# Kernel optimization log

Measured on AMD Instinct MI355X. Metric: run time of the kernel, lower is better.

## Reference

```python
import jax, jax.numpy as jnp
import numpy as np

NUM_HEADS = 12


def setup_inputs() -> dict:
    key = jax.random.key(0)
    k1, k2, k3 = jax.random.split(key, 3)
    B, S, D = 2, 2048, 768
    x = jax.random.normal(k1, (B, S, D), dtype=jnp.float32)
    # torch Linear init: normal(std=0.002) weights, zero bias; stored as [in, out]
    W_qkv = jax.random.normal(k2, (D, 3 * D), dtype=jnp.float32) * 0.002
    b_qkv = jnp.zeros((3 * D,), dtype=jnp.float32)
    W_vw = jax.random.normal(k3, (D, D), dtype=jnp.float32) * 0.002
    b_vw = jnp.zeros((D,), dtype=jnp.float32)
    mask = jnp.ones((B, S), dtype=jnp.int32)  # padding mask, all valid
    return {"x": x, "W_qkv": W_qkv, "b_qkv": b_qkv, "W_vw": W_vw, "b_vw": b_vw, "mask": mask}


def reference(x, W_qkv, b_qkv, W_vw, b_vw, mask):
    B, S, D = x.shape
    H = NUM_HEADS
    Dh = D // H
    qkv = (x @ W_qkv + b_qkv).reshape(B, S, 3, H, Dh)
    q, k, v = qkv[:, :, 0], qkv[:, :, 1], qkv[:, :, 2]
    # [B, H, S, S] attention scores (full matrix, as in original)
    w = jnp.einsum('bshd,bzhd->bhsz', q, k)
    w = w / jnp.sqrt(jnp.asarray(Dh, dtype=x.dtype))  # scale=True
    # log-mask trick: padding mask [B,1,1,S] * causal tril [1,1,S,S]
    causal = jnp.tril(jnp.ones((S, S), dtype=x.dtype))
    wholemask = mask.astype(x.dtype)[:, None, None, :] * causal[None, None]
    w = w + jnp.log(wholemask)
    w = jax.nn.softmax(w, axis=-1)
    vw = jnp.einsum('bhsz,bzhd->bshd', w, v).reshape(B, S, D)
    return vw @ W_vw + b_vw
```

## Files before the change

### kernel.cpp

```cpp
#include <hip/hip_runtime.h>
#include <hip/hip_bf16.h>
#include <cmath>
#include <cstddef>

#define B_    2
#define S_    2048
#define D_    768
#define H_    12
#define DH_   64
#define NQKV_ 2304

typedef __attribute__((ext_vector_type(8))) short  short8;
typedef __attribute__((ext_vector_type(4))) short  short4v;
typedef __attribute__((ext_vector_type(4))) float  floatx4;

__device__ __forceinline__ unsigned short f2bf(float f) {
    union { __hip_bfloat16 h; unsigned short u; } cv;
    cv.h = __float2bfloat16(f);
    return cv.u;
}

__device__ __forceinline__ void stage16(const unsigned short* g, unsigned short* ldsbase, int lane) {
#if __has_builtin(__builtin_amdgcn_global_load_lds)
    __builtin_amdgcn_global_load_lds(
        (const __attribute__((address_space(1))) unsigned int*)g,
        (__attribute__((address_space(3))) unsigned int*)ldsbase, 16, 0, 0);
#else
    *(short8*)(ldsbase + lane * 8) = *(const short8*)g;
#endif
}

__global__ void cvt_x_kernel(const float* __restrict__ x, unsigned short* __restrict__ xb)
{
    int i = (blockIdx.x * 256 + threadIdx.x) * 8;
    float4 a = *(const float4*)(x + i);
    float4 b = *(const float4*)(x + i + 4);
    short8 v;
    v[0] = (short)f2bf(a.x); v[1] = (short)f2bf(a.y);
    v[2] = (short)f2bf(a.z); v[3] = (short)f2bf(a.w);
    v[4] = (short)f2bf(b.x); v[5] = (short)f2bf(b.y);
    v[6] = (short)f2bf(b.z); v[7] = (short)f2bf(b.w);
    *(short8*)(xb + i) = v;
}

__global__ void cvt_w_kernel(const float* __restrict__ Wq, const float* __restrict__ Wv,
                             unsigned short* __restrict__ WqT, unsigned short* __restrict__ WvT)
{
    const int z = blockIdx.z;
    const int N = z ? D_ : NQKV_;
    if ((int)blockIdx.x * 32 >= N) return;
    const float* W = z ? Wv : Wq;
    unsigned short* WT = z ? WvT : WqT;

    __shared__ float t[32][33];
    const int tx = threadIdx.x, ty = threadIdx.y;
    const int n0 = blockIdx.x * 32, k0 = blockIdx.y * 32;
    #pragma unroll
    for (int i = 0; i < 4; ++i)
        t[ty + i * 8][tx] = W[(size_t)(k0 + ty + i * 8) * N + n0 + tx];
    __syncthreads();
    #pragma unroll
    for (int i = 0; i < 4; ++i)
        WT[(size_t)(n0 + ty + i * 8) * 768 + k0 + tx] = f2bf(t[tx][ty + i * 8]);
}

__global__ void vt_kernel(const unsigned short* __restrict__ V, unsigned short* __restrict__ VT)
{
    __shared__ unsigned short t[64][72];
    const int bh = blockIdx.x, s0 = blockIdx.y * 64;
    const unsigned short* src = V + ((size_t)bh * S_ + s0) * DH_;
    const int r = threadIdx.x >> 3, c = (threadIdx.x & 7) * 8;
    #pragma unroll
    for (int it = 0; it < 2; ++it)
        *(short8*)&t[r + it * 32][c] = *(const short8*)(src + (size_t)(r + it * 32) * DH_ + c);
    __syncthreads();
    #pragma unroll
    for (int it = 0; it < 2; ++it) {
        int d = r + it * 32;
        short8 v;
        #pragma unroll
        for (int i = 0; i < 8; ++i) v[i] = (short)t[c + i][d];
        *(short8*)(VT + ((size_t)bh * DH_ + d) * S_ + s0 + c) = v;
    }
}

__global__ __launch_bounds__(256, 2)
void mm_qkv_kernel(const unsigned short* __restrict__ A, const unsigned short* __restrict__ BT,
                   const float* __restrict__ bias,
                   unsigned short* __restrict__ Qo, unsigned short* __restrict__ Ko,
                   unsigned short* __restrict__ Vo)
{
    __shared__ unsigned short As[128][32];
    __shared__ unsigned short Bs[128][32];
    const int tid = threadIdx.x;
    const int wid = tid >> 6, lane = tid & 63;
    const int q = lane >> 4, ln = lane & 15;
    const int wm = (wid & 1) * 64, wn = (wid >> 1) * 64;
    const int m0 = blockIdx.y * 128, n0 = blockIdx.x * 128;
    const int lrow = wid * 16 + (lane >> 2);
    const int lcol = (lane & 3) * 8;
    const unsigned short* Ag = A  + (size_t)(m0 + lrow) * 768 + lcol;
    const unsigned short* Bg = BT + (size_t)(n0 + lrow) * 768 + lcol;

    floatx4 acc[4][4] = {};
    for (int k0 = 0; k0 < 768; k0 += 32) {
        __syncthreads();
        stage16(Ag + k0,            &As[wid * 16][0],      lane);
        stage16(Ag + k0 + 64 * 768, &As[64 + wid * 16][0], lane);
        stage16(Bg + k0,            &Bs[wid * 16][0],      lane);
        stage16(Bg + k0 + 64 * 768, &Bs[64 + wid * 16][0], lane);
        __syncthreads();
        short8 af[4], bf[4];
        #pragma unroll
        for (int mt = 0; mt < 4; ++mt) af[mt] = *(const short8*)&As[wm + mt * 16 + ln][q * 8];
        #pragma unroll
        for (int nt = 0; nt < 4; ++nt) bf[nt] = *(const short8*)&Bs[wn + nt * 16 + ln][q * 8];
        #pragma unroll
        for (int mt = 0; mt < 4; ++mt)
            #pragma unroll
            for (int nt = 0; nt < 4; ++nt)
                acc[mt][nt] = __builtin_amdgcn_mfma_f32_16x16x32_bf16(af[mt], bf[nt], acc[mt][nt], 0, 0, 0);
    }

    const int t = n0 / 768;
    unsigned short* __restrict__ dst = (t == 0) ? Qo : ((t == 1) ? Ko : Vo);
    const float qscale = (t == 0) ? 0.18033688011112042f : 1.0f;
    const int colb = n0 - t * 768 + wn;
    float bv[4];
    #pragma unroll
    for (int nt = 0; nt < 4; ++nt) bv[nt] = bias[n0 + wn + nt * 16 + ln];
    #pragma unroll
    for (int mt = 0; mt < 4; ++mt)
        #pragma unroll
        for (int r = 0; r < 4; ++r) {
            int row = m0 + wm + mt * 16 + q * 4 + r;
            int bb = row >> 11, s = row & 2047;
            #pragma unroll
            for (int nt = 0; nt < 4; ++nt) {
                int col = colb + nt * 16 + ln;
                int h = col >> 6, d = col & 63;
                dst[((size_t)(bb * H_ + h) * S_ + s) * DH_ + d] = f2bf((acc[mt][nt][r] + bv[nt]) * qscale);
            }
        }
}

__global__ __launch_bounds__(256, 2)
void flash12_kernel(const unsigned short* __restrict__ Qg, const unsigned short* __restrict__ Kg,
                    const unsigned short* __restrict__ VTg, const int* __restrict__ mask,
                    unsigned short* __restrict__ VW)
{
    __shared__ unsigned short Ks[2][32][64];
    __shared__ unsigned short Vs[2][64][32];
    __shared__ unsigned short Pl[4][32][40];

    const int tid = threadIdx.x;
    const int wid = tid >> 6, lane = tid & 63;
    const int q = lane >> 4, ln = lane & 15;
    const int bh = blockIdx.x % 24;
    const int j  = 15 - blockIdx.x / 24;
    const int b = bh / H_, h = bh % H_;
    const int r0 = j * 128;
    const int r0w = r0 + wid * 32;
    const int T = 4 * j + 4;
    const int Lw = 4 * j + wid + 1;

    const unsigned short* Qb = Qg  + (size_t)bh * S_ * DH_;
    const unsigned short* Kb = Kg  + (size_t)bh * S_ * DH_;
    const unsigned short* Vt = VTg + (size_t)bh * DH_ * S_;
    const int* mb = mask + b * S_;

    const int krow = wid * 8 + (lane >> 3);
    const int kslt = ((lane & 7) ^ (lane >> 3)) * 8;
    const int vrow = wid * 16 + (lane >> 2);
    const int vslt = (((lane & 3) ^ ((lane >> 2) & 3))) * 8;

    short8 qf[2][2];
    #pragma unroll
    for (int rt = 0; rt < 2; ++rt)
        #pragma unroll
        for (int kk = 0; kk < 2; ++kk)
            qf[rt][kk] = *(const short8*)(Qb + (size_t)(r0w + rt * 16 + ln) * DH_ + kk * 32 + q * 8);

    floatx4 o[2][4] = {};
    float li[2] = {};

    stage16(Kb + (size_t)(krow) * DH_ + kslt,  &Ks[0][wid * 8][0],  lane);
    stage16(Vt + (size_t)(vrow) * S_  + vslt,  &Vs[0][wid * 16][0], lane);

    for (int t = 0; t < T; ++t) {
        __syncthreads();

        const int z0 = t * 32;
        const int mi = mb[z0 + (lane & 31)];

        if (t + 1 < T) {
            const int z1 = z0 + 32;
            const int nb = (t + 1) & 1;
            stage16(Kb + (size_t)(z1 + krow) * DH_ + kslt, &Ks[nb][wid * 8][0],  lane);
            stage16(Vt + (size_t)(vrow) * S_ + z1 + vslt,  &Vs[nb][wid * 16][0], lane);
        }

        if (t >= Lw) continue;
        const int cb = t & 1;

        short8 kf[2][2];
        #pragma unroll
        for (int zt = 0; zt < 2; ++zt)
            #pragma unroll
            for (int kk = 0; kk < 2; ++kk)
                kf[zt][kk] = *(const short8*)&Ks[cb][zt * 16 + ln][(((kk * 4 + q) ^ (ln & 7)) * 8)];

        short8 vb[4];
        #pragma unroll
        for (int dt = 0; dt < 4; ++dt)
            vb[dt] = *(const short8*)&Vs[cb][dt * 16 + ln][((q ^ (ln & 3)) * 8)];

        floatx4 s[2][2] = {};
        __builtin_amdgcn_s_setprio(1);
        #pragma unroll
        for (int zt = 0; zt < 2; ++zt)
            #pragma unroll
            for (int rt = 0; rt < 2; ++rt) {
                s[zt][rt] = __builtin_amdgcn_mfma_f32_16x16x32_bf16(kf[zt][0], qf[rt][0], s[zt][rt], 0, 0, 0);
                s[zt][rt] = __builtin_amdgcn_mfma_f32_16x16x32_bf16(kf[zt][1], qf[rt][1], s[zt][rt], 0, 0, 0);
            }
        __builtin_amdgcn_s_setprio(0);

        const bool diag = (t == Lw - 1);
        if (__all(mi != 0) && !diag) {
            #pragma unroll
            for (int zt = 0; zt < 2; ++zt)
                #pragma unroll
                for (int rt = 0; rt < 2; ++rt) {
                    float p0 = exp2f(s[zt][rt][0]);
                    float p1 = exp2f(s[zt][rt][1]);
                    float p2 = exp2f(s[zt][rt][2]);
                    float p3 = exp2f(s[zt][rt][3]);
                    li[rt] += (p0 + p1) + (p2 + p3);
                    short4v pk;
                    pk[0] = (short)f2bf(p0); pk[1] = (short)f2bf(p1);
                    pk[2] = (short)f2bf(p2); pk[3] = (short)f2bf(p3);
                    *(short4v*)&Pl[wid][rt * 16 + ln][zt * 16 + q * 4] = pk;
                }
        } else {
            const int4 mA = *(const int4*)&mb[z0 + q * 4];
            const int4 mB = *(const int4*)&mb[z0 + 16 + q * 4];
            int ma[2][4];
            ma[0][0] = mA.x; ma[0][1] = mA.y; ma[0][2] = mA.z; ma[0][3] = mA.w;
            ma[1][0] = mB.x; ma[1][1] = mB.y; ma[1][2] = mB.z; ma[1][3] = mB.w;
            #pragma unroll
            for (int zt = 0; zt < 2; ++zt)
                #pragma unroll
                for (int rt = 0; rt < 2; ++rt) {
                    const int zb = z0 + zt * 16 + q * 4;
                    const int r  = r0w + rt * 16 + ln;
                    float p[4];
                    #pragma unroll
                    for (int rr = 0; rr < 4; ++rr) {
                        p[rr] = exp2f(s[zt][rt][rr]);
                        if (!ma[zt][rr] || (zb + rr > r)) p[rr] = 0.0f;
                    }
                    li[rt] += (p[0] + p[1]) + (p[2] + p[3]);
                    short4v pk;
                    pk[0] = (short)f2bf(p[0]); pk[1] = (short)f2bf(p[1]);
                    pk[2] = (short)f2bf(p[2]); pk[3] = (short)f2bf(p[3]);
                    *(short4v*)&Pl[wid][rt * 16 + ln][zt * 16 + q * 4] = pk;
                }
        }

        #pragma unroll
        for (int mt = 0; mt < 2; ++mt) {
            short8 a = *(const short8*)&Pl[wid][mt * 16 + ln][q * 8];
            __builtin_amdgcn_s_setprio(1);
            #pragma unroll
            for (int dt = 0; dt < 4; ++dt)
                o[mt][dt] = __builtin_amdgcn_mfma_f32_16x16x32_bf16(a, vb[dt], o[mt][dt], 0, 0, 0);
            __builtin_amdgcn_s_setprio(0);
        }
    }

    #pragma unroll
    for (int rt = 0; rt < 2; ++rt) {
        float v = li[rt];
        v += __shfl_xor(v, 16);
        v += __shfl_xor(v, 32);
        li[rt] = v;
    }

    #pragma unroll
    for (int mt = 0; mt < 2; ++mt) {
        float inv[4];
        #pragma unroll
        for (int rr = 0; rr < 4; ++rr)
            inv[rr] = 1.0f / __shfl(li[mt], q * 4 + rr);
        #pragma unroll
        for (int rr = 0; rr < 4; ++rr) {
            int srow = r0w + mt * 16 + q * 4 + rr;
            unsigned short* dst = VW + ((size_t)b * S_ + srow) * D_ + h * DH_ + ln;
            #pragma unroll
            for (int dt = 0; dt < 4; ++dt)
                dst[dt * 16] = f2bf(o[mt][dt][rr] * inv[rr]);
        }
    }
}

__global__ __launch_bounds__(256, 2)
void mm_proj_kernel(const unsigned short* __restrict__ A, const unsigned short* __restrict__ BT,
                    const float* __restrict__ bias, float* __restrict__ C)
{
    __shared__ unsigned short As[128][32];
    __shared__ unsigned short Bs[64][32];
    const int tid = threadIdx.x;
    const int wid = tid >> 6, lane = tid & 63;
    const int q = lane >> 4, ln = lane & 15;
    const int wm = (wid & 1) * 64, wn = (wid >> 1) * 32;
    const int m0 = blockIdx.y * 128, n0 = blockIdx.x * 64;
    const int lrow = wid * 16 + (lane >> 2);
    const int lcol = (lane & 3) * 8;
    const unsigned short* Ag = A  + (size_t)(m0 + lrow) * 768 + lcol;
    const unsigned short* Bg = BT + (size_t)(n0 + lrow) * 768 + lcol;

    floatx4 acc[4][2] = {};
    for (int k0 = 0; k0 < 768; k0 += 32) {
        __syncthreads();
        stage16(Ag + k0,            &As[wid * 16][0],      lane);
        stage16(Ag + k0 + 64 * 768, &As[64 + wid * 16][0], lane);
        stage16(Bg + k0,            &Bs[wid * 16][0],      lane);
        __syncthreads();
        short8 af[4], bf[2];
        #pragma unroll
        for (int mt = 0; mt < 4; ++mt) af[mt] = *(const short8*)&As[wm + mt * 16 + ln][q * 8];
        #pragma unroll
        for (int nt = 0; nt < 2; ++nt) bf[nt] = *(const short8*)&Bs[wn + nt * 16 + ln][q * 8];
        #pragma unroll
        for (int mt = 0; mt < 4; ++mt)
            #pragma unroll
            for (int nt = 0; nt < 2; ++nt)
                acc[mt][nt] = __builtin_amdgcn_mfma_f32_16x16x32_bf16(af[mt], bf[nt], acc[mt][nt], 0, 0, 0);
    }

    float bv[2];
    #pragma unroll
    for (int nt = 0; nt < 2; ++nt) bv[nt] = bias[n0 + wn + nt * 16 + ln];
    #pragma unroll
    for (int mt = 0; mt < 4; ++mt)
        #pragma unroll
        for (int r = 0; r < 4; ++r) {
            size_t row = (size_t)m0 + wm + mt * 16 + q * 4 + r;
            #pragma unroll
            for (int nt = 0; nt < 2; ++nt)
                C[row * D_ + n0 + wn + nt * 16 + ln] = acc[mt][nt][r] + bv[nt];
        }
}

extern "C" void kernel_launch(void* const* d_in, const int* in_sizes, int n_in,
                              void* d_out, int out_size, void* d_ws, size_t ws_size,
                              hipStream_t stream)
{
    (void)in_sizes; (void)n_in; (void)out_size; (void)ws_size;
    const float* x    = (const float*)d_in[0];
    const float* Wqkv = (const float*)d_in[1];
    const float* bqkv = (const float*)d_in[2];
    const float* Wvw  = (const float*)d_in[3];
    const float* bvw  = (const float*)d_in[4];
    const int*   mask = (const int*)d_in[5];
    float* out = (float*)d_out;

    const size_t XN  = (size_t)B_ * S_ * D_;
    unsigned short* ws  = (unsigned short*)d_ws;
    unsigned short* xb  = ws;
    unsigned short* WqT = xb  + XN;
    unsigned short* WvT = WqT + (size_t)NQKV_ * D_;
    unsigned short* Qb  = WvT + (size_t)D_ * D_;
    unsigned short* Kb  = Qb + XN;
    unsigned short* Vb  = Kb + XN;
    unsigned short* VbT = Vb + XN;
    unsigned short* VW  = VbT + XN;

    cvt_x_kernel<<<dim3(XN / (256 * 8)), 256, 0, stream>>>(x, xb);
    cvt_w_kernel<<<dim3(NQKV_ / 32, D_ / 32, 2), dim3(32, 8), 0, stream>>>(Wqkv, Wvw, WqT, WvT);
    mm_qkv_kernel<<<dim3(NQKV_ / 128, (B_ * S_) / 128), 256, 0, stream>>>(xb, WqT, bqkv, Qb, Kb, Vb);
    vt_kernel<<<dim3(B_ * H_, S_ / 64), 256, 0, stream>>>(Vb, VbT);
    flash12_kernel<<<dim3(24 * 16), 256, 0, stream>>>(Qb, Kb, VbT, mask, VW);
    mm_proj_kernel<<<dim3(D_ / 64, (B_ * S_) / 128), 256, 0, stream>>>(VW, WvT, bvw, out);
}
```

Baseline: 190.2 us.

## Split attention block into 8 waves with triple-buffered K/V prefetch

The flash attention kernel now runs 512 threads per block, and each wave owns 16 query rows instead of 32. Waves 0-3 stage K while waves 4-7 stage V. K/V tiles are triple-buffered with a two-tile lookahead, synchronised by a manual vmcnt wait plus s_barrier instead of __syncthreads. The per-tile padding-mask check is replaced by one all-valid scan up front. The aim is more latency hiding and less load and barrier serialisation per tile, at the cost of more LDS, more per-block synchronisation and a smaller MFMA working set per wave.

Result: faster. 182.5 us (-4.0%).

```diff
diff --git a/kernel.cpp b/kernel.cpp
--- a/kernel.cpp
+++ b/kernel.cpp
@@ -144,14 +144,14 @@
         }
 }
 
-__global__ __launch_bounds__(256, 2)
-void flash12_kernel(const unsigned short* __restrict__ Qg, const unsigned short* __restrict__ Kg,
+__global__ __launch_bounds__(512, 2)
+void flash13_kernel(const unsigned short* __restrict__ Qg, const unsigned short* __restrict__ Kg,
                     const unsigned short* __restrict__ VTg, const int* __restrict__ mask,
                     unsigned short* __restrict__ VW)
 {
-    __shared__ unsigned short Ks[2][32][64];
-    __shared__ unsigned short Vs[2][64][32];
-    __shared__ unsigned short Pl[4][32][40];
+    __shared__ unsigned short Ks[3][32][64];
+    __shared__ unsigned short Vs[3][64][32];
+    __shared__ unsigned short Pl[8][16][40];
 
     const int tid = threadIdx.x;
     const int wid = tid >> 6, lane = tid & 63;
@@ -159,49 +159,69 @@
     const int bh = blockIdx.x % 24;
     const int j  = 15 - blockIdx.x / 24;
     const int b = bh / H_, h = bh % H_;
-    const int r0 = j * 128;
-    const int r0w = r0 + wid * 32;
-    const int T = 4 * j + 4;
-    const int Lw = 4 * j + wid + 1;
+    const int r0w = j * 128 + wid * 16;
+    const int T  = 4 * j + 4;
+    const int Lw = 4 * j + (wid >> 1) + 1;
 
     const unsigned short* Qb = Qg  + (size_t)bh * S_ * DH_;
     const unsigned short* Kb = Kg  + (size_t)bh * S_ * DH_;
     const unsigned short* Vt = VTg + (size_t)bh * DH_ * S_;
     const int* mb = mask + b * S_;
 
-    const int krow = wid * 8 + (lane >> 3);
+    const bool isK = (wid < 4);
+    const int krow = (wid & 3) * 8 + (lane >> 3);
     const int kslt = ((lane & 7) ^ (lane >> 3)) * 8;
-    const int vrow = wid * 16 + (lane >> 2);
-    const int vslt = (((lane & 3) ^ ((lane >> 2) & 3))) * 8;
-
-    short8 qf[2][2];
-    #pragma unroll
-    for (int rt = 0; rt < 2; ++rt)
-        #pragma unroll
-        for (int kk = 0; kk < 2; ++kk)
-            qf[rt][kk] = *(const short8*)(Qb + (size_t)(r0w + rt * 16 + ln) * DH_ + kk * 32 + q * 8);
-
-    floatx4 o[2][4] = {};
-    float li[2] = {};
-
-    stage16(Kb + (size_t)(krow) * DH_ + kslt,  &Ks[0][wid * 8][0],  lane);
-    stage16(Vt + (size_t)(vrow) * S_  + vslt,  &Vs[0][wid * 16][0], lane);
+    const int vrow = (wid & 3) * 16 + (lane >> 2);
+    const int vslt = ((lane & 3) ^ ((lane >> 2) & 3)) * 8;
+
+    short8 qf[2];
+    #pragma unroll
+    for (int kk = 0; kk < 2; ++kk)
+        qf[kk] = *(const short8*)(Qb + (size_t)(r0w + ln) * DH_ + kk * 32 + q * 8);
+
+    int am = 1;
+    for (int zz = 0; zz < T * 32; zz += 512) {
+        int v[8];
+        #pragma unroll
+        for (int u = 0; u < 8; ++u) {
+            int z = zz + u * 64 + lane;
+            v[u] = (z < T * 32) ? mb[z] : 1;
+        }
+        #pragma unroll
+        for (int u = 0; u < 8; ++u) am &= (v[u] != 0);
+    }
+    const bool allmask = __all(am != 0);
+
+    asm volatile("" ::: "memory");
+
+    if (isK) {
+        stage16(Kb + (size_t)(0 * 32 + krow) * DH_ + kslt, &Ks[0][(wid & 3) * 8][0], lane);
+        stage16(Kb + (size_t)(1 * 32 + krow) * DH_ + kslt, &Ks[1][(wid & 3) * 8][0], lane);
+    } else {
+        stage16(Vt + (size_t)vrow * S_ + 0 * 32 + vslt, &Vs[0][(wid & 3) * 16][0], lane);
+        stage16(Vt + (size_t)vrow * S_ + 1 * 32 + vslt, &Vs[1][(wid & 3) * 16][0], lane);
+    }
+
+    floatx4 o[4] = {};
+    float li = 0.0f;
 
     for (int t = 0; t < T; ++t) {
-        __syncthreads();
-
+        asm volatile("s_waitcnt vmcnt(1)" ::: "memory");
+        __builtin_amdgcn_s_barrier();
+        __builtin_amdgcn_sched_barrier(0);
+
+        {
+            const int ts = (t + 2 < T) ? (t + 2) : (T - 1);
+            int wb = ts - (ts / 3) * 3;
+            if (isK)
+                stage16(Kb + (size_t)(ts * 32 + krow) * DH_ + kslt, &Ks[wb][(wid & 3) * 8][0], lane);
+            else
+                stage16(Vt + (size_t)vrow * S_ + ts * 32 + vslt, &Vs[wb][(wid & 3) * 16][0], lane);
+        }
+
+        if (t >= Lw) continue;
+        const int cb = t - (t / 3) * 3;
         const int z0 = t * 32;
-        const int mi = mb[z0 + (lane & 31)];
-
-        if (t + 1 < T) {
-            const int z1 = z0 + 32;
-            const int nb = (t + 1) & 1;
-            stage16(Kb + (size_t)(z1 + krow) * DH_ + kslt, &Ks[nb][wid * 8][0],  lane);
-            stage16(Vt + (size_t)(vrow) * S_ + z1 + vslt,  &Vs[nb][wid * 16][0], lane);
-        }
-
-        if (t >= Lw) continue;
-        const int cb = t & 1;
 
         short8 kf[2][2];
         #pragma unroll
@@ -215,33 +235,29 @@
         for (int dt = 0; dt < 4; ++dt)
             vb[dt] = *(const short8*)&Vs[cb][dt * 16 + ln][((q ^ (ln & 3)) * 8)];
 
-        floatx4 s[2][2] = {};
+        floatx4 s[2] = {};
         __builtin_amdgcn_s_setprio(1);
         #pragma unroll
-        for (int zt = 0; zt < 2; ++zt)
-            #pragma unroll
-            for (int rt = 0; rt < 2; ++rt) {
-                s[zt][rt] = __builtin_amdgcn_mfma_f32_16x16x32_bf16(kf[zt][0], qf[rt][0], s[zt][rt], 0, 0, 0);
-                s[zt][rt] = __builtin_amdgcn_mfma_f32_16x16x32_bf16(kf[zt][1], qf[rt][1], s[zt][rt], 0, 0, 0);
+        for (int zt = 0; zt < 2; ++zt) {
+            s[zt] = __builtin_amdgcn_mfma_f32_16x16x32_bf16(kf[zt][0], qf[0], s[zt], 0, 0, 0);
+            s[zt] = __builtin_amdgcn_mfma_f32_16x16x32_bf16(kf[zt][1], qf[1], s[zt], 0, 0, 0);
+        }
+        __builtin_amdgcn_s_setprio(0);
+
+        const bool diag = (t == Lw - 1);
+        if (allmask && !diag) {
+            #pragma unroll
+            for (int zt = 0; zt < 2; ++zt) {
+                float p0 = exp2f(s[zt][0]);
+                float p1 = exp2f(s[zt][1]);
+                float p2 = exp2f(s[zt][2]);
+                float p3 = exp2f(s[zt][3]);
+                li += (p0 + p1) + (p2 + p3);
+                short4v pk;
+                pk[0] = (short)f2bf(p0); pk[1] = (short)f2bf(p1);
+                pk[2] = (short)f2bf(p2); pk[3] = (short)f2bf(p3);
+                *(short4v*)&Pl[wid][ln][zt * 16 + q * 4] = pk;
             }
-        __builtin_amdgcn_s_setprio(0);
-
-        const bool diag = (t == Lw - 1);
-        if (__all(mi != 0) && !diag) {
-            #pragma unroll
-            for (int zt = 0; zt < 2; ++zt)
-                #pragma unroll
-                for (int rt = 0; rt < 2; ++rt) {
-                    float p0 = exp2f(s[zt][rt][0]);
-                    float p1 = exp2f(s[zt][rt][1]);
-                    float p2 = exp2f(s[zt][rt][2]);
-                    float p3 = exp2f(s[zt][rt][3]);
-                    li[rt] += (p0 + p1) + (p2 + p3);
-                    short4v pk;
-                    pk[0] = (short)f2bf(p0); pk[1] = (short)f2bf(p1);
-                    pk[2] = (short)f2bf(p2); pk[3] = (short)f2bf(p3);
-                    *(short4v*)&Pl[wid][rt * 16 + ln][zt * 16 + q * 4] = pk;
-                }
         } else {
             const int4 mA = *(const int4*)&mb[z0 + q * 4];
             const int4 mB = *(const int4*)&mb[z0 + 16 + q * 4];
@@ -249,58 +265,47 @@
             ma[0][0] = mA.x; ma[0][1] = mA.y; ma[0][2] = mA.z; ma[0][3] = mA.w;
             ma[1][0] = mB.x; ma[1][1] = mB.y; ma[1][2] = mB.z; ma[1][3] = mB.w;
             #pragma unroll
-            for (int zt = 0; zt < 2; ++zt)
+            for (int zt = 0; zt < 2; ++zt) {
+                const int zb = z0 + zt * 16 + q * 4;
+                const int r  = r0w + ln;
+                float p[4];
                 #pragma unroll
-                for (int rt = 0; rt < 2; ++rt) {
-                    const int zb = z0 + zt * 16 + q * 4;
-                    const int r  = r0w + rt * 16 + ln;
-                    float p[4];
-                    #pragma unroll
-                    for (int rr = 0; rr < 4; ++rr) {
-                        p[rr] = exp2f(s[zt][rt][rr]);
-                        if (!ma[zt][rr] || (zb + rr > r)) p[rr] = 0.0f;
-                    }
-                    li[rt] += (p[0] + p[1]) + (p[2] + p[3]);
-                    short4v pk;
-                    pk[0] = (short)f2bf(p[0]); pk[1] = (short)f2bf(p[1]);
-                    pk[2] = (short)f2bf(p[2]); pk[3] = (short)f2bf(p[3]);
-                    *(short4v*)&Pl[wid][rt * 16 + ln][zt * 16 + q * 4] = pk;
+                for (int rr = 0; rr < 4; ++rr) {
+                    p[rr] = exp2f(s[zt][rr]);
+                    if (!ma[zt][rr] || (zb + rr > r)) p[rr] = 0.0f;
                 }
-        }
-
-        #pragma unroll
-        for (int mt = 0; mt < 2; ++mt) {
-            short8 a = *(const short8*)&Pl[wid][mt * 16 + ln][q * 8];
+                li += (p[0] + p[1]) + (p[2] + p[3]);
+                short4v pk;
+                pk[0] = (short)f2bf(p[0]); pk[1] = (short)f2bf(p[1]);
+                pk[2] = (short)f2bf(p[2]); pk[3] = (short)f2bf(p[3]);
+                *(short4v*)&Pl[wid][ln][zt * 16 + q * 4] = pk;
+            }
+        }
+
+        {
+            short8 a = *(const short8*)&Pl[wid][ln][q * 8];
             __builtin_amdgcn_s_setprio(1);
             #pragma unroll
             for (int dt = 0; dt < 4; ++dt)
-                o[mt][dt] = __builtin_amdgcn_mfma_f32_16x16x32_bf16(a, vb[dt], o[mt][dt], 0, 0, 0);
+                o[dt] = __builtin_amdgcn_mfma_f32_16x16x32_bf16(a, vb[dt], o[dt], 0, 0, 0);
             __builtin_amdgcn_s_setprio(0);
         }
     }
 
-    #pragma unroll
-    for (int rt = 0; rt < 2; ++rt) {
-        float v = li[rt];
-        v += __shfl_xor(v, 16);
-        v += __shfl_xor(v, 32);
-        li[rt] = v;
-    }
-
-    #pragma unroll
-    for (int mt = 0; mt < 2; ++mt) {
-        float inv[4];
-        #pragma unroll
-        for (int rr = 0; rr < 4; ++rr)
-            inv[rr] = 1.0f / __shfl(li[mt], q * 4 + rr);
-        #pragma unroll
-        for (int rr = 0; rr < 4; ++rr) {
-            int srow = r0w + mt * 16 + q * 4 + rr;
-            unsigned short* dst = VW + ((size_t)b * S_ + srow) * D_ + h * DH_ + ln;
-            #pragma unroll
-            for (int dt = 0; dt < 4; ++dt)
-                dst[dt * 16] = f2bf(o[mt][dt][rr] * inv[rr]);
-        }
+    li += __shfl_xor(li, 16);
+    li += __shfl_xor(li, 32);
+
+    float inv[4];
+    #pragma unroll
+    for (int rr = 0; rr < 4; ++rr)
+        inv[rr] = 1.0f / __shfl(li, q * 4 + rr);
+    #pragma unroll
+    for (int rr = 0; rr < 4; ++rr) {
+        int srow = r0w + q * 4 + rr;
+        unsigned short* dst = VW + ((size_t)b * S_ + srow) * D_ + h * DH_ + ln;
+        #pragma unroll
+        for (int dt = 0; dt < 4; ++dt)
+            dst[dt * 16] = f2bf(o[dt][rr] * inv[rr]);
     }
 }
 
@@ -381,6 +386,6 @@
     cvt_w_kernel<<<dim3(NQKV_ / 32, D_ / 32, 2), dim3(32, 8), 0, stream>>>(Wqkv, Wvw, WqT, WvT);
     mm_qkv_kernel<<<dim3(NQKV_ / 128, (B_ * S_) / 128), 256, 0, stream>>>(xb, WqT, bqkv, Qb, Kb, Vb);
     vt_kernel<<<dim3(B_ * H_, S_ / 64), 256, 0, stream>>>(Vb, VbT);
-    flash12_kernel<<<dim3(24 * 16), 256, 0, stream>>>(Qb, Kb, VbT, mask, VW);
+    flash13_kernel<<<dim3(24 * 16), 512, 0, stream>>>(Qb, Kb, VbT, mask, VW);
     mm_proj_kernel<<<dim3(D_ / 64, (B_ * S_) / 128), 256, 0, stream>>>(VW, WvT, bvw, out);
 }
```
